# Kernel tuning notes

Measured on AMD Instinct MI355X. Metric: run time of the kernel, lower is better.

## Reference

```python
import jax, jax.numpy as jnp
import numpy as np

# ---- dims (match init_kwargs / mamba_ssm Mamba2 defaults) ----
VOCAB = 32000
D_MODEL = 256
N_LAYERS = 2
D_STATE = 64   # N
D_CONV = 4
EXPAND = 2
MAX_SEQ = 1024
HEADDIM = 64   # P (Mamba2 default)
D_INNER = EXPAND * D_MODEL            # 512
NHEADS = D_INNER // HEADDIM           # 8
CONV_DIM = D_INNER + 2 * D_STATE      # 640 (ngroups=1)
D_IN_PROJ = 2 * D_INNER + 2 * D_STATE + NHEADS  # 1160
B, L = 2, 1024
EPS = 1e-5


def setup_inputs() -> dict:
    key = jax.random.key(0)
    ks = jax.random.split(key, 16)
    s = 0.02
    input_ids = jax.random.randint(ks[0], (B, L), 0, VOCAB)
    attention_mask = jnp.ones((B, L), jnp.float32)
    tok_emb = jax.random.normal(ks[1], (VOCAB, D_MODEL)) * s
    tok_emb = tok_emb.at[0].set(0.0)  # padding_idx=0
    pos_emb = jax.random.normal(ks[2], (MAX_SEQ, D_MODEL)) * s
    # per-direction (2) x per-layer (N_LAYERS) stacked Mamba2 params
    shp = (2, N_LAYERS)
    in_proj_w = jax.random.normal(ks[3], shp + (D_IN_PROJ, D_MODEL)) * s
    conv_w = jax.random.normal(ks[4], shp + (CONV_DIM, D_CONV)) * 0.1
    conv_b = jnp.zeros(shp + (CONV_DIM,))
    dt = jax.random.uniform(ks[5], shp + (NHEADS,), minval=1e-3, maxval=1e-1)
    dt_bias = dt + jnp.log(-jnp.expm1(-dt))  # inverse softplus
    A_log = jnp.log(jax.random.uniform(ks[6], shp + (NHEADS,), minval=1.0, maxval=16.0))
    D_param = jnp.ones(shp + (NHEADS,))
    norm_w = jnp.ones(shp + (D_INNER,))
    out_proj_w = jax.random.normal(ks[7], shp + (D_MODEL, D_INNER)) * s
    fusion_w = jax.random.normal(ks[8], (2 * D_MODEL, 2 * D_MODEL)) * s
    fusion_b = jnp.zeros((2 * D_MODEL,))
    ln_w = jnp.ones((D_MODEL,))
    ln_b = jnp.zeros((D_MODEL,))
    return dict(input_ids=input_ids, attention_mask=attention_mask,
                tok_emb=tok_emb, pos_emb=pos_emb, in_proj_w=in_proj_w,
                conv_w=conv_w, conv_b=conv_b, dt_bias=dt_bias, A_log=A_log,
                D_param=D_param, norm_w=norm_w, out_proj_w=out_proj_w,
                fusion_w=fusion_w, fusion_b=fusion_b, ln_w=ln_w, ln_b=ln_b)


def _mamba2_layer(u, in_w, cw, cb, dtb, A_log, Dp, nw, ow):
    """One Mamba2 block forward; u: (B,L,D_MODEL)."""
    bsz, seqlen, _ = u.shape
    zxbcdt = u @ in_w.T                                   # (B,L,1160)
    z = zxbcdt[..., :D_INNER]
    xBC = zxbcdt[..., D_INNER:D_INNER + CONV_DIM]
    dt = jax.nn.softplus(zxbcdt[..., D_INNER + CONV_DIM:] + dtb)  # (B,L,H)
    # causal depthwise conv over time + SiLU
    xc = jax.lax.conv_general_dilated(
        xBC.transpose(0, 2, 1), cw[:, None, :], (1,), [(D_CONV - 1, 0)],
        feature_group_count=CONV_DIM, dimension_numbers=('NCH', 'OIH', 'NCH'))
    xBC = jax.nn.silu(xc.transpose(0, 2, 1) + cb)
    x = xBC[..., :D_INNER].reshape(bsz, seqlen, NHEADS, HEADDIM)  # (B,L,H,P)
    Bm = xBC[..., D_INNER:D_INNER + D_STATE]                      # (B,L,N)
    Cm = xBC[..., D_INNER + D_STATE:]                             # (B,L,N)
    A = -jnp.exp(A_log)                                           # (H,)

    def step(h, inp):
        x_t, B_t, C_t, dt_t = inp          # (B,H,P),(B,N),(B,N),(B,H)
        dA = jnp.exp(dt_t * A)             # (B,H)
        h = h * dA[:, :, None, None] \
            + (dt_t[:, :, None] * x_t)[..., None] * B_t[:, None, None, :]
        y_t = jnp.einsum('bhpn,bn->bhp', h, C_t)
        return h, y_t

    h0 = jnp.zeros((bsz, NHEADS, HEADDIM, D_STATE), u.dtype)
    xs = (x.transpose(1, 0, 2, 3), Bm.transpose(1, 0, 2),
          Cm.transpose(1, 0, 2), dt.transpose(1, 0, 2))
    _, ys = jax.lax.scan(step, h0, xs)                 # (L,B,H,P)
    y = ys.transpose(1, 0, 2, 3) + Dp[None, None, :, None] * x
    y = y.reshape(bsz, seqlen, D_INNER)
    # gated RMSNorm (norm_before_gate=False)
    y = y * jax.nn.silu(z)
    y = y * jax.lax.rsqrt(jnp.mean(y * y, -1, keepdims=True) + EPS) * nw
    return y @ ow.T


def _stack(h, params, d):
    (in_w, cw, cb, dtb, alog, Dp, nw, ow) = params
    for i in range(N_LAYERS):
        h = _mamba2_layer(h, in_w[d, i], cw[d, i], cb[d, i], dtb[d, i],
                          alog[d, i], Dp[d, i], nw[d, i], ow[d, i])
    return h


def reference(input_ids, attention_mask, tok_emb, pos_emb, in_proj_w, conv_w,
              conv_b, dt_bias, A_log, D_param, norm_w, out_proj_w,
              fusion_w, fusion_b, ln_w, ln_b):
    bsz, seqlen = input_ids.shape
    h = tok_emb[input_ids] + pos_emb[:seqlen][None]        # (B,L,D)
    h = h * attention_mask[..., None]                      # dropout = identity (eval)
    params = (in_proj_w, conv_w, conv_b, dt_bias, A_log, D_param, norm_w, out_proj_w)
    fwd = _stack(h, params, 0)
    bwd = jnp.flip(_stack(jnp.flip(h, 1), params, 1), 1)
    combined = jnp.concatenate([fwd, bwd], -1)             # (B,L,2D)
    gate = jax.nn.sigmoid(combined @ fusion_w.T + fusion_b)
    gf, gb = gate[..., :D_MODEL], gate[..., D_MODEL:]
    fused = gf * fwd + gb * bwd
    mu = jnp.mean(fused, -1, keepdims=True)
    var = jnp.mean((fused - mu) ** 2, -1, keepdims=True)
    return (fused - mu) * jax.lax.rsqrt(var + EPS) * ln_w + ln_b
```

## Files before the change

kernel.cpp:

```cpp
#include <hip/hip_runtime.h>
#include <cstddef>

#define LSEQ    1024
#define DMODEL  256
#define DINNER  512
#define DSTATE  64
#define NHEADS  8
#define HEADDIM 64
#define CONVDIM 640
#define DINPROJ 1160
#define ROWS    2048
#define EPSF    1e-5f
#define NC      32
#define LC      32
#define XBCW    648
#define HROW    131072

#define WIN  593920
#define WOUT 262144
#define WF   262144
#define PSI  296960
#define PSO  131072
#define LSTRIDE 1712128
#define WTOTAL  1974272
#define WBLOCKS 1928

typedef _Float16 f16;
typedef f16   v8h __attribute__((ext_vector_type(8)));
typedef f16   v4h __attribute__((ext_vector_type(4)));
typedef float v4f __attribute__((ext_vector_type(4)));
#define MFMA16(a, b, c) __builtin_amdgcn_mfma_f32_16x16x32_f16(a, b, c, 0, 0, 0)

__device__ __forceinline__ float sigmoidf_(float x) { return 1.0f / (1.0f + expf(-x)); }
__device__ __forceinline__ float siluf_(float x)    { return x / (1.0f + expf(-x)); }
__device__ __forceinline__ float softplusf_(float x) {
    return x > 0.0f ? x + log1pf(expf(-x)) : log1pf(expf(x));
}
__device__ __forceinline__ void split16(float v, f16& h, f16& l) {
    h = (f16)v;
    l = (f16)((v - (float)h) * 4096.0f);
}

__device__ __forceinline__ float4 conv4_(const float* __restrict__ xbcd,
                                         const float* __restrict__ cwl,
                                         const float* __restrict__ cbl,
                                         int base, int tg, int ch0) {
    float4 acc = *(const float4*)&cbl[ch0];
    float4 cw0 = *(const float4*)&cwl[(ch0 + 0) * 4];
    float4 cw1 = *(const float4*)&cwl[(ch0 + 1) * 4];
    float4 cw2 = *(const float4*)&cwl[(ch0 + 2) * 4];
    float4 cw3 = *(const float4*)&cwl[(ch0 + 3) * 4];
    const float* w0 = (const float*)&cw0;
    const float* w1 = (const float*)&cw1;
    const float* w2 = (const float*)&cw2;
    const float* w3 = (const float*)&cw3;
#pragma unroll
    for (int k = 0; k < 4; ++k) {
        int ts = tg - 3 + k;
        if (ts >= 0) {
            float4 xv = *(const float4*)&xbcd[(size_t)(base + ts) * XBCW + ch0];
            acc.x = fmaf(xv.x, w0[k], acc.x);
            acc.y = fmaf(xv.y, w1[k], acc.y);
            acc.z = fmaf(xv.z, w2[k], acc.z);
            acc.w = fmaf(xv.w, w3[k], acc.w);
        }
    }
    return acc;
}

__global__ __launch_bounds__(256) void prep_kernel(
    const int* __restrict__ ids, const float* __restrict__ mask,
    const float* __restrict__ tok, const float* __restrict__ pos,
    f16* __restrict__ uh, f16* __restrict__ ul,
    const float* __restrict__ inw, const float* __restrict__ ow, const float* __restrict__ fw,
    f16* __restrict__ wb) {
    int blk = blockIdx.x;
    if (blk < ROWS) {
        int row = blk;
        int d = threadIdx.x;
        int b = row >> 10, t = row & 1023;
        int id = ids[row];
        float v = tok[(size_t)id * DMODEL + d] + pos[(size_t)t * DMODEL + d];
        v *= mask[row];
        f16 h, l; split16(v, h, l);
        size_t fwd = (size_t)row * DMODEL + d;
        size_t bwd = (size_t)ROWS * DMODEL + ((size_t)(b << 10) + (1023 - t)) * DMODEL + d;
        uh[fwd] = h; ul[fwd] = l;
        uh[bwd] = h; ul[bwd] = l;
    } else {
        int idx = ((blk - ROWS) * 256 + threadIdx.x) * 4;
#pragma unroll
        for (int e = idx; e < idx + 4; ++e) {
            if (e >= WTOTAL) break;
            float v; f16 *dh, *dl; int off;
            if (e < 2 * (WIN + WOUT)) {
                int layer = e / (WIN + WOUT);
                int r = e - layer * (WIN + WOUT);
                if (r < WIN) {
                    int d = r / PSI, rr = r - d * PSI;
                    v = inw[(size_t)(d * 2 + layer) * PSI + rr];
                    dh = wb + (size_t)layer * LSTRIDE; dl = dh + WIN; off = r;
                } else {
                    int r2 = r - WIN;
                    int d = r2 / PSO, rr = r2 - d * PSO;
                    v = ow[(size_t)(d * 2 + layer) * PSO + rr];
                    dh = wb + (size_t)layer * LSTRIDE + 2 * WIN; dl = dh + WOUT; off = r2;
                }
            } else {
                int e3 = e - 2 * (WIN + WOUT);
                v = fw[e3];
                dh = wb + 2 * (size_t)LSTRIDE; dl = dh + WF; off = e3;
            }
            f16 h, l; split16(v, h, l);
            dh[off] = h; dl[off] = l;
        }
    }
}

__global__ __launch_bounds__(256) void gemm_f16x3(
    const f16* __restrict__ Ah, const f16* __restrict__ Al, long sA,
    const f16* __restrict__ Wh, const f16* __restrict__ Wl, long sW,
    int N, int K, int Nsplit,
    float* __restrict__ O0, int ld0, long sO0,
    float* __restrict__ O1, int ld1, long sO1,
    f16* __restrict__ Ph, f16* __restrict__ Pl, int ldP, long sP,
    int has32, int haspair, int flipcomb) {
    int dir = blockIdx.z;
    Ah += (size_t)dir * sA; Al += (size_t)dir * sA;
    Wh += (size_t)dir * sW; Wl += (size_t)dir * sW;
    if (has32)  { O0 += (size_t)dir * sO0; O1 += (size_t)dir * sO1; }
    if (haspair){ Ph += (size_t)dir * sP;  Pl += (size_t)dir * sP; }

    __shared__ f16 sm[4 * 64 * 72];
    f16* As_h = sm;
    f16* As_l = sm + 64 * 72;
    f16* Ws_h = sm + 2 * 64 * 72;
    f16* Ws_l = sm + 3 * 64 * 72;

    int tid = threadIdx.x;
    int m0 = blockIdx.x * 64, n0 = blockIdx.y * 64;
    int srow = tid >> 2, sseg = tid & 3;
    int lane = tid & 63, w = tid >> 6;
    int wrow = (w >> 1) * 32, wcol = (w & 1) * 32;
    int q = lane >> 4, r16 = lane & 15;
    bool wok = (n0 + srow) < N;

    v4f accM[2][2], accX[2][2];
#pragma unroll
    for (int i = 0; i < 2; ++i)
#pragma unroll
        for (int j = 0; j < 2; ++j) { accM[i][j] = (v4f)0.0f; accX[i][j] = (v4f)0.0f; }

    float4 ah0, ah1, al0, al1, wh0, wh1, wl0, wl1;
    {
        size_t aoff = (size_t)(m0 + srow) * K + sseg * 16;
        ah0 = *(const float4*)&Ah[aoff];
        ah1 = *(const float4*)&Ah[aoff + 8];
        al0 = *(const float4*)&Al[aoff];
        al1 = *(const float4*)&Al[aoff + 8];
        wh0 = make_float4(0.f,0.f,0.f,0.f); wh1 = wh0; wl0 = wh0; wl1 = wh0;
        if (wok) {
            size_t woff = (size_t)(n0 + srow) * K + sseg * 16;
            wh0 = *(const float4*)&Wh[woff];
            wh1 = *(const float4*)&Wh[woff + 8];
            wl0 = *(const float4*)&Wl[woff];
            wl1 = *(const float4*)&Wl[woff + 8];
        }
    }

    for (int k0 = 0; k0 < K; k0 += 64) {
        __syncthreads();
        int d = srow * 72 + sseg * 16;
        *(float4*)&As_h[d] = ah0; *(float4*)&As_h[d + 8] = ah1;
        *(float4*)&As_l[d] = al0; *(float4*)&As_l[d + 8] = al1;
        *(float4*)&Ws_h[d] = wh0; *(float4*)&Ws_h[d + 8] = wh1;
        *(float4*)&Ws_l[d] = wl0; *(float4*)&Ws_l[d + 8] = wl1;
        __syncthreads();

        if (k0 + 64 < K) {
            size_t aoff = (size_t)(m0 + srow) * K + (k0 + 64) + sseg * 16;
            ah0 = *(const float4*)&Ah[aoff];
            ah1 = *(const float4*)&Ah[aoff + 8];
            al0 = *(const float4*)&Al[aoff];
            al1 = *(const float4*)&Al[aoff + 8];
            if (wok) {
                size_t woff = (size_t)(n0 + srow) * K + (k0 + 64) + sseg * 16;
                wh0 = *(const float4*)&Wh[woff];
                wh1 = *(const float4*)&Wh[woff + 8];
                wl0 = *(const float4*)&Wl[woff];
                wl1 = *(const float4*)&Wl[woff + 8];
            }
        }

#pragma unroll
        for (int ks = 0; ks < 64; ks += 32) {
            v8h fa_h[2], fa_l[2], fb_h[2], fb_l[2];
#pragma unroll
            for (int i = 0; i < 2; ++i) {
                int ra = (wrow + i * 16 + r16) * 72 + ks + q * 8;
                int rb = (wcol + i * 16 + r16) * 72 + ks + q * 8;
                fa_h[i] = *(const v8h*)&As_h[ra];
                fa_l[i] = *(const v8h*)&As_l[ra];
                fb_h[i] = *(const v8h*)&Ws_h[rb];
                fb_l[i] = *(const v8h*)&Ws_l[rb];
            }
#pragma unroll
            for (int i = 0; i < 2; ++i)
#pragma unroll
                for (int j = 0; j < 2; ++j) {
                    accM[i][j] = MFMA16(fa_h[i], fb_h[j], accM[i][j]);
                    accX[i][j] = MFMA16(fa_h[i], fb_l[j], accX[i][j]);
                    accX[i][j] = MFMA16(fa_l[i], fb_h[j], accX[i][j]);
                }
        }
    }

    const float cs = 1.0f / 4096.0f;
#pragma unroll
    for (int i = 0; i < 2; ++i)
#pragma unroll
        for (int j = 0; j < 2; ++j) {
            int nn = n0 + wcol + j * 16 + r16;
            if (nn < N) {
#pragma unroll
                for (int r = 0; r < 4; ++r) {
                    float v = accM[i][j][r] + accX[i][j][r] * cs;
                    int mm = m0 + wrow + i * 16 + q * 4 + r;
                    if (has32) {
                        if (nn < Nsplit) O0[(size_t)mm * ld0 + nn] = v;
                        else             O1[(size_t)mm * ld1 + (nn - Nsplit)] = v;
                    }
                    if (haspair) {
                        f16 h, l; split16(v, h, l);
                        if (flipcomb) {
                            int bb = mm >> 10, tt_ = mm & 1023;
                            size_t drow = dir == 0 ? (size_t)mm : (size_t)((bb << 10) + (1023 - tt_));
                            size_t dcol = dir == 0 ? (size_t)nn : (size_t)(nn + 256);
                            Ph[drow * 512 + dcol] = h;
                            Pl[drow * 512 + dcol] = l;
                        } else {
                            Ph[(size_t)mm * ldP + nn] = h;
                            Pl[(size_t)mm * ldP + nn] = l;
                        }
                    }
                }
            }
        }
}

__global__ __launch_bounds__(256) void scan_chunk_kernel(
    const float* __restrict__ xbc, const float* __restrict__ cw, const float* __restrict__ cb,
    const float* __restrict__ dtb, float* __restrict__ y,
    const float* __restrict__ Alog, const float* __restrict__ Dp,
    float* __restrict__ H, float* __restrict__ cumb, float* __restrict__ Cbuf, int layer) {
    __shared__ f16 Chs[32 * 72], Cls[32 * 72], Bhs[32 * 72], Bls[32 * 72];
    __shared__ f16 Xth[64 * 40], Xtl[64 * 40];
    __shared__ f16 Bvh[64 * 40], Bvl[64 * 40];
    __shared__ f16 Gph[32 * 40], Gpl[32 * 40];
    __shared__ float sLC[32], sRD[32], sV[32];

    int blk = blockIdx.x;
    int u = blk >> 5, c = blk & 31;
    int dir = u >> 4, b = (u >> 3) & 1, h = u & 7;
    int tid = threadIdx.x;
    int w = tid >> 6, lane = tid & 63;
    int pi = dir * 2 + layer;
    float Av = -expf(Alog[pi * NHEADS + h]);
    float Dv = Dp[pi * NHEADS + h];
    const float* xbcd = xbc + (size_t)dir * ROWS * XBCW;
    const float* cwl = cw + (size_t)pi * CONVDIM * 4;
    const float* cbl = cb + (size_t)pi * CONVDIM;
    float dtbh = dtb[pi * NHEADS + h];
    float* yd = y + (size_t)dir * ROWS * DINNER;
    int t0 = c * LC, base = b << 10;
    const float cs = 1.0f / 4096.0f;

    if (w == 0) {
        int tp = lane & 31;
        float dtraw = xbcd[(size_t)(base + t0 + tp) * XBCW + CONVDIM + h];
        float dt_l = softplusf_(dtraw + dtbh);
        float dA_l = expf(dt_l * Av);
        float cum_l = dA_l;
#pragma unroll
        for (int off = 1; off < 32; off <<= 1) {
            float o = __shfl_up(cum_l, off);
            if (tp >= off) cum_l *= o;
        }
        float lclast = __shfl(cum_l, 31);
        if (lane < 32) {
            cumb[(u << 10) + t0 + lane] = cum_l;
            float rl = 1.0f / cum_l;
            sLC[lane] = cum_l;
            sRD[lane] = rl * dt_l;
            sV[lane]  = lclast * rl * dt_l * 4096.0f;
        }
    }
    __syncthreads();

#pragma unroll
    for (int j = 0; j < 4; ++j) {
        int idx = j * 256 + tid;
        int tr = idx >> 5, c4 = idx & 31;
        int ch0 = 512 + c4 * 4;
        float4 a = conv4_(xbcd, cwl, cbl, base, t0 + tr, ch0);
        float e[4] = {siluf_(a.x), siluf_(a.y), siluf_(a.z), siluf_(a.w)};
        float vs = sV[tr];
        f16 hq[4], lq[4];
#pragma unroll
        for (int k = 0; k < 4; ++k) split16(e[k], hq[k], lq[k]);
        int col0 = c4 * 4;
        if (col0 < 64) {
            *(v4h*)&Bhs[tr * 72 + col0] = *(v4h*)hq;
            *(v4h*)&Bls[tr * 72 + col0] = *(v4h*)lq;
#pragma unroll
            for (int k = 0; k < 4; ++k) {
                f16 h2, l2; split16(e[k] * vs, h2, l2);
                Bvh[(col0 + k) * 40 + tr] = h2;
                Bvl[(col0 + k) * 40 + tr] = l2;
            }
        } else {
            *(v4h*)&Chs[tr * 72 + col0 - 64] = *(v4h*)hq;
            *(v4h*)&Cls[tr * 72 + col0 - 64] = *(v4h*)lq;
            if (h == 0)
                *(float4*)&Cbuf[((size_t)dir * ROWS + base + t0 + tr) * 64 + (col0 - 64)] =
                    make_float4(e[0], e[1], e[2], e[3]);
        }
    }
#pragma unroll
    for (int j = 0; j < 2; ++j) {
        int idx = j * 256 + tid;
        int sr = idx >> 4, c4 = idx & 15;
        int ch0 = h * HEADDIM + c4 * 4;
        float4 a = conv4_(xbcd, cwl, cbl, base, t0 + sr, ch0);
        float e[4] = {siluf_(a.x), siluf_(a.y), siluf_(a.z), siluf_(a.w)};
#pragma unroll
        for (int k = 0; k < 4; ++k) {
            f16 hh, ll; split16(e[k], hh, ll);
            Xth[(c4 * 4 + k) * 40 + sr] = hh;
            Xtl[(c4 * 4 + k) * 40 + sr] = ll;
        }
    }
    __syncthreads();

    int q = lane >> 4, r16 = lane & 15;

    {
        int ti = w >> 1, si = w & 1;
        v4f gM = (v4f)0.0f, gX = (v4f)0.0f;
#pragma unroll
        for (int ks = 0; ks < 64; ks += 32) {
            int ra = (ti * 16 + r16) * 72 + ks + q * 8;
            int rb = (si * 16 + r16) * 72 + ks + q * 8;
            v8h ca  = *(const v8h*)&Chs[ra];
            v8h cl2 = *(const v8h*)&Cls[ra];
            v8h ba  = *(const v8h*)&Bhs[rb];
            v8h bl2 = *(const v8h*)&Bls[rb];
            gM = MFMA16(ca, ba, gM);
            gX = MFMA16(ca, bl2, gX);
            gX = MFMA16(cl2, ba, gX);
        }
#pragma unroll
        for (int r = 0; r < 4; ++r) {
            int t = ti * 16 + q * 4 + r;
            int s = si * 16 + r16;
            float g = gM[r] + gX[r] * cs;
            float wgt = (s <= t) ? sLC[t] * sRD[s] * 4096.0f : 0.0f;
            f16 hh, ll; split16(g * wgt, hh, ll);
            Gph[t * 40 + s] = hh;
            Gpl[t * 40 + s] = ll;
        }
    }
    __syncthreads();

    {
        int ti = w >> 1;
        int ra = (ti * 16 + r16) * 40 + q * 8;
        v8h ga = *(const v8h*)&Gph[ra];
        v8h gl = *(const v8h*)&Gpl[ra];
#pragma unroll
        for (int jj = 0; jj < 2; ++jj) {
            int pj = (w & 1) * 2 + jj;
            int rb = (pj * 16 + r16) * 40 + q * 8;
            v8h xa = *(const v8h*)&Xth[rb];
            v8h xl = *(const v8h*)&Xtl[rb];
            v4f m = (v4f)0.0f, x2 = (v4f)0.0f;
            m  = MFMA16(ga, xa, m);
            x2 = MFMA16(ga, xl, x2);
            x2 = MFMA16(gl, xa, x2);
#pragma unroll
            for (int r = 0; r < 4; ++r) {
                int t = ti * 16 + q * 4 + r;
                int pp = pj * 16 + r16;
                float xv = (float)Xth[pp * 40 + t] + cs * (float)Xtl[pp * 40 + t];
                float val = (m[r] + x2[r] * cs) * cs + Dv * xv;
                yd[(size_t)(base + t0 + t) * DINNER + h * HEADDIM + pp] = val;
            }
        }
    }

    {
        float* Hb = H + (size_t)c * HROW + (size_t)u * 4096;
        int ni = w;
        int ra = (ni * 16 + r16) * 40 + q * 8;
        v8h ba  = *(const v8h*)&Bvh[ra];
        v8h bl2 = *(const v8h*)&Bvl[ra];
#pragma unroll
        for (int pj = 0; pj < 4; ++pj) {
            int rb = (pj * 16 + r16) * 40 + q * 8;
            v8h xa = *(const v8h*)&Xth[rb];
            v8h xl = *(const v8h*)&Xtl[rb];
            v4f m = (v4f)0.0f, x2 = (v4f)0.0f;
            m  = MFMA16(ba, xa, m);
            x2 = MFMA16(ba, xl, x2);
            x2 = MFMA16(bl2, xa, x2);
#pragma unroll
            for (int r = 0; r < 4; ++r) {
                int n = ni * 16 + q * 4 + r;
                int pp = pj * 16 + r16;
                Hb[pp * 64 + n] = (m[r] + x2[r] * cs) * cs;
            }
        }
    }
}

__global__ __launch_bounds__(256) void carry_kernel(
    float* __restrict__ H, const float* __restrict__ cumb) {
    int blk = blockIdx.x;
    int u = blk >> 4;
    int e = ((blk & 15) << 8) + threadIdx.x;
    size_t off = (size_t)u * 4096 + e;
    float carry = 0.f;
#pragma unroll 4
    for (int c = 0; c < NC; ++c) {
        float Pc = cumb[(u << 10) + c * LC + (LC - 1)];
        float* p = H + (size_t)c * HROW + off;
        float ev = *p;
        *p = carry;
        carry = fmaf(Pc, carry, ev);
    }
}

__global__ __launch_bounds__(128) void fix_kernel(
    const float* __restrict__ Cbuf, float* __restrict__ y,
    const float* __restrict__ H, const float* __restrict__ cumb) {
    __shared__ float sC[LC * 64];
    __shared__ float sCum[LC];
    int blk = blockIdx.x;
    int u = blk / (NC - 1);
    int c = blk % (NC - 1) + 1;
    int dir = u >> 4, b = (u >> 3) & 1, h = u & 7;
    int tid = threadIdx.x;
    int w = tid >> 6, p = tid & 63;
    const float* Cb = Cbuf + (size_t)dir * ROWS * 64;
    float* yd = y + (size_t)dir * ROWS * DINNER;
    int t0 = c * LC, base = b << 10;
    if (tid < LC) sCum[tid] = cumb[(u << 10) + t0 + tid];
#pragma unroll
    for (int j = 0; j < 4; ++j) {
        int f4 = j * 128 + tid;
        int trow = f4 >> 4, col4 = f4 & 15;
        float4 v = *(const float4*)&Cb[(size_t)(base + t0 + trow) * 64 + col4 * 4];
        *(float4*)&sC[trow * 64 + col4 * 4] = v;
    }
    const float* Hb = H + (size_t)c * HROW + (size_t)u * 4096 + p * 64;
    float hin[DSTATE];
#pragma unroll
    for (int n = 0; n < DSTATE; n += 4) {
        float4 v = *(const float4*)&Hb[n];
        hin[n] = v.x; hin[n + 1] = v.y; hin[n + 2] = v.z; hin[n + 3] = v.w;
    }
    __syncthreads();
#pragma unroll 2
    for (int tt = w * 16; tt < w * 16 + 16; ++tt) {
        float cumt = sCum[tt];
        const float* Cs = &sC[tt * 64];
        float y0 = 0.f, y1 = 0.f, y2 = 0.f, y3 = 0.f;
#pragma unroll
        for (int n = 0; n < DSTATE; n += 4) {
            y0 = fmaf(hin[n],     Cs[n],     y0);
            y1 = fmaf(hin[n + 1], Cs[n + 1], y1);
            y2 = fmaf(hin[n + 2], Cs[n + 2], y2);
            y3 = fmaf(hin[n + 3], Cs[n + 3], y3);
        }
        size_t yi = (size_t)(base + t0 + tt) * DINNER + h * HEADDIM + p;
        yd[yi] += cumt * ((y0 + y1) + (y2 + y3));
    }
}

__global__ __launch_bounds__(256) void gate_rms_kernel(
    const float* __restrict__ y, const float* __restrict__ zbuf,
    const float* __restrict__ nw, f16* __restrict__ yh, f16* __restrict__ yl, int layer) {
    int row = blockIdx.x;
    int dir = blockIdx.y;
    const float* zrow = zbuf + ((size_t)dir * ROWS + row) * DINNER;
    const float* yrow = y + ((size_t)dir * ROWS + row) * DINNER;
    f16* yhr = yh + ((size_t)dir * ROWS + row) * DINNER;
    f16* ylr = yl + ((size_t)dir * ROWS + row) * DINNER;
    const float* nwl = nw + (dir * 2 + layer) * DINNER;
    int tid = threadIdx.x;
    int i0 = tid, i1 = tid + 256;
    float g0 = yrow[i0] * siluf_(zrow[i0]);
    float g1 = yrow[i1] * siluf_(zrow[i1]);
    __shared__ float red[256];
    red[tid] = fmaf(g0, g0, g1 * g1);
    __syncthreads();
    for (int s = 128; s > 0; s >>= 1) {
        if (tid < s) red[tid] += red[tid + s];
        __syncthreads();
    }
    float scale = 1.0f / sqrtf(red[0] / (float)DINNER + EPSF);
    float v0 = g0 * scale * nwl[i0];
    float v1 = g1 * scale * nwl[i1];
    f16 h, l;
    split16(v0, h, l); yhr[i0] = h; ylr[i0] = l;
    split16(v1, h, l); yhr[i1] = h; ylr[i1] = l;
}

__global__ __launch_bounds__(256) void fusion_ln2_kernel(
    const float* __restrict__ u32, const float* __restrict__ gate,
    const float* __restrict__ fb, const float* __restrict__ lnw,
    const float* __restrict__ lnb, float* __restrict__ out) {
    int row = blockIdx.x;
    int b = row >> 10, t = row & 1023;
    int tid = threadIdx.x;
    float f  = u32[(size_t)row * DMODEL + tid];
    float bw = u32[(size_t)ROWS * DMODEL + ((size_t)(b << 10) + (1023 - t)) * DMODEL + tid];
    float g0 = sigmoidf_(gate[(size_t)row * 512 + tid] + fb[tid]);
    float g1 = sigmoidf_(gate[(size_t)row * 512 + 256 + tid] + fb[256 + tid]);
    float fused = g0 * f + g1 * bw;
    __shared__ float red[256];
    red[tid] = fused;
    __syncthreads();
    for (int s = 128; s > 0; s >>= 1) {
        if (tid < s) red[tid] += red[tid + s];
        __syncthreads();
    }
    float mu = red[0] / (float)DMODEL;
    __syncthreads();
    float d = fused - mu;
    red[tid] = d * d;
    __syncthreads();
    for (int s = 128; s > 0; s >>= 1) {
        if (tid < s) red[tid] += red[tid + s];
        __syncthreads();
    }
    float var = red[0] / (float)DMODEL;
    out[(size_t)row * DMODEL + tid] = d * (1.0f / sqrtf(var + EPSF)) * lnw[tid] + lnb[tid];
}

extern "C" void kernel_launch(void* const* d_in, const int* in_sizes, int n_in,
                              void* d_out, int out_size, void* d_ws, size_t ws_size,
                              hipStream_t stream) {
    const int*   ids  = (const int*)d_in[0];
    const float* mask = (const float*)d_in[1];
    const float* tok  = (const float*)d_in[2];
    const float* pos  = (const float*)d_in[3];
    const float* inw  = (const float*)d_in[4];
    const float* cw   = (const float*)d_in[5];
    const float* cb   = (const float*)d_in[6];
    const float* dtb  = (const float*)d_in[7];
    const float* alog = (const float*)d_in[8];
    const float* dpar = (const float*)d_in[9];
    const float* nw   = (const float*)d_in[10];
    const float* ow   = (const float*)d_in[11];
    const float* fw   = (const float*)d_in[12];
    const float* fb   = (const float*)d_in[13];
    const float* lnw  = (const float*)d_in[14];
    const float* lnb  = (const float*)d_in[15];

    float* ws = (float*)d_ws;
    float* zbuf = ws;
    float* xbc  = ws +  2097152;
    float* ybuf = ws +  4751360;
    f16*   yh   = (f16*)(ws +  6848512);
    f16*   yl   = (f16*)(ws +  7897088);
    float* gate = ws +  8945664;
    f16*   uh   = (f16*)(ws +  9994240);
    f16*   ul   = (f16*)(ws + 11042816);
    f16*   wb   = (f16*)(ws + 12091392);
    float* H    = ws + 14065664;
    float* cumb = ws + 18259968;
    float* Cbuf = ws + 18292736;
    float* u32  = ybuf;
    f16*   combh = (f16*)(ybuf + 1048576);
    f16*   combl = (f16*)(ybuf + 1572864);
    f16*   wfh = wb + 2 * (size_t)LSTRIDE;
    f16*   wfl = wfh + WF;

    prep_kernel<<<ROWS + WBLOCKS, 256, 0, stream>>>(ids, mask, tok, pos, uh, ul, inw, ow, fw, wb);

    for (int layer = 0; layer < 2; ++layer) {
        f16* wih = wb + (size_t)layer * LSTRIDE;
        f16* wil = wih + WIN;
        f16* woh = wb + (size_t)layer * LSTRIDE + 2 * WIN;
        f16* wol = woh + WOUT;

        dim3 g1(ROWS / 64, (DINPROJ + 63) / 64, 2);
        gemm_f16x3<<<g1, 256, 0, stream>>>(
            uh, ul, (long)ROWS * DMODEL,
            wih, wil, (long)PSI,
            DINPROJ, DMODEL, DINNER,
            zbuf, DINNER, (long)ROWS * DINNER,
            xbc, XBCW, (long)ROWS * XBCW,
            (f16*)nullptr, (f16*)nullptr, 0, 0L,
            1, 0, 0);

        scan_chunk_kernel<<<32 * NC, 256, 0, stream>>>(
            xbc, cw, cb, dtb, ybuf, alog, dpar, H, cumb, Cbuf, layer);
        carry_kernel<<<32 * 16, 256, 0, stream>>>(H, cumb);
        fix_kernel<<<32 * (NC - 1), 128, 0, stream>>>(Cbuf, ybuf, H, cumb);
        gate_rms_kernel<<<dim3(ROWS, 2), 256, 0, stream>>>(ybuf, zbuf, nw, yh, yl, layer);

        dim3 g2(ROWS / 64, DMODEL / 64, 2);
        if (layer == 0) {
            gemm_f16x3<<<g2, 256, 0, stream>>>(
                yh, yl, (long)ROWS * DINNER,
                woh, wol, (long)PSO,
                DMODEL, DINNER, DMODEL,
                u32, DMODEL, (long)ROWS * DMODEL,
                u32, DMODEL, (long)ROWS * DMODEL,
                uh, ul, DMODEL, (long)ROWS * DMODEL,
                1, 1, 0);
        } else {
            gemm_f16x3<<<g2, 256, 0, stream>>>(
                yh, yl, (long)ROWS * DINNER,
                woh, wol, (long)PSO,
                DMODEL, DINNER, DMODEL,
                u32, DMODEL, (long)ROWS * DMODEL,
                u32, DMODEL, (long)ROWS * DMODEL,
                combh, combl, 512, 0L,
                1, 1, 1);
        }
    }

    dim3 g3(ROWS / 64, 512 / 64, 1);
    gemm_f16x3<<<g3, 256, 0, stream>>>(
        combh, combl, 0L,
        wfh, wfl, 0L,
        512, 512, 512,
        gate, 512, 0L,
        gate, 512, 0L,
        (f16*)nullptr, (f16*)nullptr, 0, 0L,
        1, 0, 0);

    fusion_ln2_kernel<<<ROWS, 256, 0, stream>>>(u32, gate, fb, lnw, lnb, (float*)d_out);
}
```

Before: 287.4 us.

## Precompute B/C conv+SiLU once per layer and use wave-shuffle reductions

Adds a separate kernel that computes the causal conv and SiLU for the shared B and C channels once per direction and row, storing them in a buffer. Previously every head block of the scan recomputed them. The scan and fix kernels now read this buffer, and the scan no longer writes C itself. The RMS-norm and LayerNorm reductions switch from shared-memory tree loops to wavefront shuffles with a 4-entry cross-wave combine, cutting barriers. The cost is one extra kernel launch and an extra global round trip for the B/C buffer.

```diff
diff --git a/kernel.cpp b/kernel.cpp
--- a/kernel.cpp
+++ b/kernel.cpp
@@ -117,6 +117,23 @@
     }
 }
 
+__global__ __launch_bounds__(256) void conv_bc_kernel(
+    const float* __restrict__ xbc, const float* __restrict__ cw, const float* __restrict__ cb,
+    float* __restrict__ BCbuf, int layer) {
+    int idx = blockIdx.x * 256 + threadIdx.x;
+    int c4 = idx & 31;
+    int row = (idx >> 5) & 2047;
+    int dir = idx >> 16;
+    int b = row >> 10, t = row & 1023;
+    const float* xbcd = xbc + (size_t)dir * ROWS * XBCW;
+    int pi = dir * 2 + layer;
+    const float* cwl = cw + (size_t)pi * CONVDIM * 4;
+    const float* cbl = cb + (size_t)pi * CONVDIM;
+    float4 a = conv4_(xbcd, cwl, cbl, b << 10, t, 512 + c4 * 4);
+    float4 e = make_float4(siluf_(a.x), siluf_(a.y), siluf_(a.z), siluf_(a.w));
+    *(float4*)&BCbuf[((size_t)dir * ROWS + row) * 128 + c4 * 4] = e;
+}
+
 __global__ __launch_bounds__(256) void gemm_f16x3(
     const f16* __restrict__ Ah, const f16* __restrict__ Al, long sA,
     const f16* __restrict__ Wh, const f16* __restrict__ Wl, long sW,
@@ -249,10 +266,11 @@
 }
 
 __global__ __launch_bounds__(256) void scan_chunk_kernel(
-    const float* __restrict__ xbc, const float* __restrict__ cw, const float* __restrict__ cb,
+    const float* __restrict__ xbc, const float* __restrict__ BCbuf,
+    const float* __restrict__ cw, const float* __restrict__ cb,
     const float* __restrict__ dtb, float* __restrict__ y,
     const float* __restrict__ Alog, const float* __restrict__ Dp,
-    float* __restrict__ H, float* __restrict__ cumb, float* __restrict__ Cbuf, int layer) {
+    float* __restrict__ H, float* __restrict__ cumb, int layer) {
     __shared__ f16 Chs[32 * 72], Cls[32 * 72], Bhs[32 * 72], Bls[32 * 72];
     __shared__ f16 Xth[64 * 40], Xtl[64 * 40];
     __shared__ f16 Bvh[64 * 40], Bvl[64 * 40];
@@ -268,6 +286,7 @@
     float Av = -expf(Alog[pi * NHEADS + h]);
     float Dv = Dp[pi * NHEADS + h];
     const float* xbcd = xbc + (size_t)dir * ROWS * XBCW;
+    const float* BCb = BCbuf + (size_t)dir * ROWS * 128;
     const float* cwl = cw + (size_t)pi * CONVDIM * 4;
     const float* cbl = cb + (size_t)pi * CONVDIM;
     float dtbh = dtb[pi * NHEADS + h];
@@ -301,9 +320,8 @@
     for (int j = 0; j < 4; ++j) {
         int idx = j * 256 + tid;
         int tr = idx >> 5, c4 = idx & 31;
-        int ch0 = 512 + c4 * 4;
-        float4 a = conv4_(xbcd, cwl, cbl, base, t0 + tr, ch0);
-        float e[4] = {siluf_(a.x), siluf_(a.y), siluf_(a.z), siluf_(a.w)};
+        float4 v = *(const float4*)&BCb[(size_t)(base + t0 + tr) * 128 + c4 * 4];
+        float e[4] = {v.x, v.y, v.z, v.w};
         float vs = sV[tr];
         f16 hq[4], lq[4];
 #pragma unroll
@@ -321,9 +339,6 @@
         } else {
             *(v4h*)&Chs[tr * 72 + col0 - 64] = *(v4h*)hq;
             *(v4h*)&Cls[tr * 72 + col0 - 64] = *(v4h*)lq;
-            if (h == 0)
-                *(float4*)&Cbuf[((size_t)dir * ROWS + base + t0 + tr) * 64 + (col0 - 64)] =
-                    make_float4(e[0], e[1], e[2], e[3]);
         }
     }
 #pragma unroll
@@ -441,7 +456,7 @@
 }
 
 __global__ __launch_bounds__(128) void fix_kernel(
-    const float* __restrict__ Cbuf, float* __restrict__ y,
+    const float* __restrict__ BCbuf, float* __restrict__ y,
     const float* __restrict__ H, const float* __restrict__ cumb) {
     __shared__ float sC[LC * 64];
     __shared__ float sCum[LC];
@@ -451,7 +466,7 @@
     int dir = u >> 4, b = (u >> 3) & 1, h = u & 7;
     int tid = threadIdx.x;
     int w = tid >> 6, p = tid & 63;
-    const float* Cb = Cbuf + (size_t)dir * ROWS * 64;
+    const float* Cb = BCbuf + (size_t)dir * ROWS * 128;
     float* yd = y + (size_t)dir * ROWS * DINNER;
     int t0 = c * LC, base = b << 10;
     if (tid < LC) sCum[tid] = cumb[(u << 10) + t0 + tid];
@@ -459,7 +474,7 @@
     for (int j = 0; j < 4; ++j) {
         int f4 = j * 128 + tid;
         int trow = f4 >> 4, col4 = f4 & 15;
-        float4 v = *(const float4*)&Cb[(size_t)(base + t0 + trow) * 64 + col4 * 4];
+        float4 v = *(const float4*)&Cb[(size_t)(base + t0 + trow) * 128 + 64 + col4 * 4];
         *(float4*)&sC[trow * 64 + col4 * 4] = v;
     }
     const float* Hb = H + (size_t)c * HROW + (size_t)u * 4096 + p * 64;
@@ -501,14 +516,14 @@
     int i0 = tid, i1 = tid + 256;
     float g0 = yrow[i0] * siluf_(zrow[i0]);
     float g1 = yrow[i1] * siluf_(zrow[i1]);
-    __shared__ float red[256];
-    red[tid] = fmaf(g0, g0, g1 * g1);
-    __syncthreads();
-    for (int s = 128; s > 0; s >>= 1) {
-        if (tid < s) red[tid] += red[tid + s];
-        __syncthreads();
-    }
-    float scale = 1.0f / sqrtf(red[0] / (float)DINNER + EPSF);
+    float s = fmaf(g0, g0, g1 * g1);
+#pragma unroll
+    for (int off = 32; off >= 1; off >>= 1) s += __shfl_down(s, off);
+    __shared__ float ws4[4];
+    if ((tid & 63) == 0) ws4[tid >> 6] = s;
+    __syncthreads();
+    float tot = (ws4[0] + ws4[1]) + (ws4[2] + ws4[3]);
+    float scale = 1.0f / sqrtf(tot / (float)DINNER + EPSF);
     float v0 = g0 * scale * nwl[i0];
     float v1 = g1 * scale * nwl[i1];
     f16 h, l;
@@ -528,23 +543,21 @@
     float g0 = sigmoidf_(gate[(size_t)row * 512 + tid] + fb[tid]);
     float g1 = sigmoidf_(gate[(size_t)row * 512 + 256 + tid] + fb[256 + tid]);
     float fused = g0 * f + g1 * bw;
-    __shared__ float red[256];
-    red[tid] = fused;
-    __syncthreads();
-    for (int s = 128; s > 0; s >>= 1) {
-        if (tid < s) red[tid] += red[tid + s];
-        __syncthreads();
-    }
-    float mu = red[0] / (float)DMODEL;
-    __syncthreads();
+    __shared__ float ws4[4];
+    float s = fused;
+#pragma unroll
+    for (int off = 32; off >= 1; off >>= 1) s += __shfl_down(s, off);
+    if ((tid & 63) == 0) ws4[tid >> 6] = s;
+    __syncthreads();
+    float mu = ((ws4[0] + ws4[1]) + (ws4[2] + ws4[3])) / (float)DMODEL;
     float d = fused - mu;
-    red[tid] = d * d;
-    __syncthreads();
-    for (int s = 128; s > 0; s >>= 1) {
-        if (tid < s) red[tid] += red[tid + s];
-        __syncthreads();
-    }
-    float var = red[0] / (float)DMODEL;
+    float s2 = d * d;
+#pragma unroll
+    for (int off = 32; off >= 1; off >>= 1) s2 += __shfl_down(s2, off);
+    __syncthreads();
+    if ((tid & 63) == 0) ws4[tid >> 6] = s2;
+    __syncthreads();
+    float var = ((ws4[0] + ws4[1]) + (ws4[2] + ws4[3])) / (float)DMODEL;
     out[(size_t)row * DMODEL + tid] = d * (1.0f / sqrtf(var + EPSF)) * lnw[tid] + lnb[tid];
 }
 
@@ -580,7 +593,7 @@
     f16*   wb   = (f16*)(ws + 12091392);
     float* H    = ws + 14065664;
     float* cumb = ws + 18259968;
-    float* Cbuf = ws + 18292736;
+    float* BCbuf= ws + 18292736;
     float* u32  = ybuf;
     f16*   combh = (f16*)(ybuf + 1048576);
     f16*   combl = (f16*)(ybuf + 1572864);
@@ -605,10 +618,11 @@
             (f16*)nullptr, (f16*)nullptr, 0, 0L,
             1, 0, 0);
 
+        conv_bc_kernel<<<512, 256, 0, stream>>>(xbc, cw, cb, BCbuf, layer);
         scan_chunk_kernel<<<32 * NC, 256, 0, stream>>>(
-            xbc, cw, cb, dtb, ybuf, alog, dpar, H, cumb, Cbuf, layer);
+            xbc, BCbuf, cw, cb, dtb, ybuf, alog, dpar, H, cumb, layer);
         carry_kernel<<<32 * 16, 256, 0, stream>>>(H, cumb);
-        fix_kernel<<<32 * (NC - 1), 128, 0, stream>>>(Cbuf, ybuf, H, cumb);
+        fix_kernel<<<32 * (NC - 1), 128, 0, stream>>>(BCbuf, ybuf, H, cumb);
         gate_rms_kernel<<<dim3(ROWS, 2), 256, 0, stream>>>(ybuf, zbuf, nw, yh, yl, layer);
 
         dim3 g2(ROWS / 64, DMODEL / 64, 2);
```

Result: no change. 285.9 us (-0.5%).
